# Kernel tuning notes

Measured on AMD Instinct MI355X. Metric: run time of the kernel, lower is better.

Reference implementation:

```python
import jax, jax.numpy as jnp
import numpy as np

U, I, D, E = 8192, 8192, 64, 1048576  # users, items, emb dim, nnz of adjacency


def spmm(row, col, val, x, n):
    """Sparse (COO) @ dense: y[r] += val * x[c], like torch.sparse.mm."""
    return jax.ops.segment_sum(val[:, None] * x[col], row, num_segments=n)


def setup_inputs() -> dict:
    key = jax.random.key(0)
    k1, k2, k3, k4, k5, k6 = jax.random.split(key, 6)
    users_emb = jax.random.normal(k1, (U, D), dtype=jnp.float32) * 0.1  # nn.init.normal_(std=0.1)
    items_emb = jax.random.normal(k2, (I, D), dtype=jnp.float32) * 0.1
    edge_row = jax.random.randint(k3, (E,), 0, U + I, dtype=jnp.int32)
    edge_col = jax.random.randint(k4, (E,), 0, U + I, dtype=jnp.int32)
    # positive normalized adjacency values (stand-in for D^-1/2 A D^-1/2 entries)
    edge_val = jax.random.uniform(k5, (E,), dtype=jnp.float32) / 64.0
    # sparse 0/1 interaction matrix densified, as in labels = interaction_mat.toarray()
    labels = (jax.random.uniform(k6, (U, I)) < 0.02).astype(jnp.float32)
    return {"users_emb": users_emb, "items_emb": items_emb,
            "edge_row": edge_row, "edge_col": edge_col,
            "edge_val": edge_val, "labels": labels, "n_layers": 3}


def reference(users_emb, items_emb, edge_row, edge_col, edge_val, labels, n_layers):
    n = users_emb.shape[0] + items_emb.shape[0]
    u = users_emb.shape[0]
    all_emb = jnp.concatenate([users_emb, items_emb], axis=0)  # [n, D]
    # stack + mean over (n_layers+1) layer outputs == online accumulation
    acc = all_emb
    for _ in range(n_layers):
        all_emb = spmm(edge_row, edge_col, edge_val, all_emb, n)
        acc = acc + all_emb
    light_out = acc / jnp.float32(n_layers + 1)
    user_emb = light_out[:u]   # [U, D]
    item_emb = light_out[u:]   # [I, D]
    scores = user_emb @ item_emb.T  # [U, I]
    # BCEWithLogitsLoss (mean reduction): logaddexp(0, s) - s*y
    loss = jnp.mean(jnp.logaddexp(jnp.float32(0.0), scores) - scores * labels)
    return (loss, user_emb, item_emb)
```

## Files before the change

### kernel.cpp

```cpp
#include <hip/hip_runtime.h>

#define U_N 8192
#define N_N 16384
#define E_N 1048576
#define CAP 128
#define CSTRIDE 16

typedef __attribute__((ext_vector_type(8)))  short short8;
typedef __attribute__((ext_vector_type(16))) float f32x16;


__device__ __forceinline__ float bfu(ushort u) {
    union { unsigned v; float f; } c; c.v = (unsigned)u << 16; return c.f;
}
__device__ __forceinline__ ushort f2bf(float f) {
    union { float f; unsigned u; } c; c.f = f;
    return (ushort)((c.u + 0x7fffu + ((c.u >> 16) & 1u)) >> 16);
}
__device__ __forceinline__ void gload_lds16(const void* g, void* l) {
    __builtin_amdgcn_global_load_lds(
        (const __attribute__((address_space(1))) void*)g,
        (__attribute__((address_space(3))) void*)l, 16, 0, 0);
}

__global__ void k_prep(const float* __restrict__ ue, const float* __restrict__ ie,
                       ushort* __restrict__ xb, float* __restrict__ acc,
                       unsigned* __restrict__ cnt) {
    int i = blockIdx.x * blockDim.x + threadIdx.x;
    const int HU = U_N * 64 / 4;
    float4 v = (i < HU) ? ((const float4*)ue)[i] : ((const float4*)ie)[i - HU];
    ((float4*)acc)[i] = v;
    ushort4 b;
    b.x = f2bf(v.x); b.y = f2bf(v.y); b.z = f2bf(v.z); b.w = f2bf(v.w);
    ((ushort4*)xb)[i] = b;
    if (i < 65536) ((uint4*)cnt)[i] = make_uint4(0, 0, 0, 0);
}

__global__ void k_bucket(const int* __restrict__ row, const int* __restrict__ col,
                         const float* __restrict__ val, unsigned* __restrict__ cnt,
                         int2* __restrict__ buckets) {
    int e = blockIdx.x * blockDim.x + threadIdx.x;
    if (e < E_N) {
        int r = row[e];
        unsigned p = atomicAdd(&cnt[r * CSTRIDE], 1u);
        if (p < CAP) buckets[(size_t)r * CAP + p] = make_int2(col[e], __float_as_int(val[e]));
    }
}

__global__ void k_spmm(const unsigned* __restrict__ cnt, const int4* __restrict__ bk4,
                       const ushort* __restrict__ x, ushort* __restrict__ xo,
                       float* __restrict__ acc) {
    int wave = (int)((blockIdx.x * blockDim.x + threadIdx.x) >> 6);
    int lane = threadIdx.x & 63;
    if (wave >= N_N) return;
    int n = (int)cnt[wave * CSTRIDE]; n = n > CAP ? CAP : n;
    const int4* bp = bk4 + (size_t)wave * (CAP / 2);
    float a = 0.f;
    int j = 0;
    for (; j + 8 <= n; j += 8) {
        int4 q0 = bp[j / 2 + 0], q1 = bp[j / 2 + 1];
        int4 q2 = bp[j / 2 + 2], q3 = bp[j / 2 + 3];
        float x0 = bfu(x[q0.x * 64 + lane]), x1 = bfu(x[q0.z * 64 + lane]);
        float x2 = bfu(x[q1.x * 64 + lane]), x3 = bfu(x[q1.z * 64 + lane]);
        float x4 = bfu(x[q2.x * 64 + lane]), x5 = bfu(x[q2.z * 64 + lane]);
        float x6 = bfu(x[q3.x * 64 + lane]), x7 = bfu(x[q3.z * 64 + lane]);
        a = fmaf(__int_as_float(q0.y), x0, a); a = fmaf(__int_as_float(q0.w), x1, a);
        a = fmaf(__int_as_float(q1.y), x2, a); a = fmaf(__int_as_float(q1.w), x3, a);
        a = fmaf(__int_as_float(q2.y), x4, a); a = fmaf(__int_as_float(q2.w), x5, a);
        a = fmaf(__int_as_float(q3.y), x6, a); a = fmaf(__int_as_float(q3.w), x7, a);
    }
    const int2* bp2 = (const int2*)bp;
    for (; j < n; ++j) {
        int2 q = bp2[j];
        a = fmaf(__int_as_float(q.y), bfu(x[q.x * 64 + lane]), a);
    }
    int idx = wave * 64 + lane;
    xo[idx] = f2bf(a);
    acc[idx] += a;
}

__global__ void k_spmm_last(const unsigned* __restrict__ cnt, const int4* __restrict__ bk4,
                            const ushort* __restrict__ x, const float* __restrict__ acc,
                            float* __restrict__ o, ushort* __restrict__ bfemb) {
    int wave = (int)((blockIdx.x * blockDim.x + threadIdx.x) >> 6);
    int lane = threadIdx.x & 63;
    if (wave >= N_N) return;
    int n = (int)cnt[wave * CSTRIDE]; n = n > CAP ? CAP : n;
    const int4* bp = bk4 + (size_t)wave * (CAP / 2);
    float a = 0.f;
    int j = 0;
    for (; j + 8 <= n; j += 8) {
        int4 q0 = bp[j / 2 + 0], q1 = bp[j / 2 + 1];
        int4 q2 = bp[j / 2 + 2], q3 = bp[j / 2 + 3];
        float x0 = bfu(x[q0.x * 64 + lane]), x1 = bfu(x[q0.z * 64 + lane]);
        float x2 = bfu(x[q1.x * 64 + lane]), x3 = bfu(x[q1.z * 64 + lane]);
        float x4 = bfu(x[q2.x * 64 + lane]), x5 = bfu(x[q2.z * 64 + lane]);
        float x6 = bfu(x[q3.x * 64 + lane]), x7 = bfu(x[q3.z * 64 + lane]);
        a = fmaf(__int_as_float(q0.y), x0, a); a = fmaf(__int_as_float(q0.w), x1, a);
        a = fmaf(__int_as_float(q1.y), x2, a); a = fmaf(__int_as_float(q1.w), x3, a);
        a = fmaf(__int_as_float(q2.y), x4, a); a = fmaf(__int_as_float(q2.w), x5, a);
        a = fmaf(__int_as_float(q3.y), x6, a); a = fmaf(__int_as_float(q3.w), x7, a);
    }
    const int2* bp2 = (const int2*)bp;
    for (; j < n; ++j) {
        int2 q = bp2[j];
        a = fmaf(__int_as_float(q.y), bfu(x[q.x * 64 + lane]), a);
    }
    int idx = wave * 64 + lane;
    float l = (acc[idx] + a) * 0.25f;
    o[idx] = l;
    bfemb[idx] = f2bf(l);
}

__global__ __launch_bounds__(256) void k_gemm_loss(const ushort* __restrict__ bfemb,
                                                   const float* __restrict__ labels,
                                                   float* __restrict__ partials) {
    __shared__ float lab[128 * 128];
    int tid  = threadIdx.x;
    int lane = tid & 63;
    int w    = tid >> 6;
    int wr   = w >> 1, wc = w & 1;
    int row0t = blockIdx.y * 128, col0t = blockIdx.x * 128;
    int row0 = row0t + wr * 64;
    int col0 = col0t + wc * 64;

    {
        int colo = (lane & 31) * 4;
        int rowo = lane >> 5;
        const float* gbase = labels + (size_t)row0t * 8192 + col0t + colo;
        #pragma unroll
        for (int t = 0; t < 16; ++t) {
            int cid = w * 16 + t;
            gload_lds16(gbase + (size_t)(cid * 2 + rowo) * 8192, &lab[cid * 256]);
        }
    }

    int lrow = lane & 31;
    int lk   = (lane >> 5) * 8;
    short8 a[2][4], b[2][4];
    #pragma unroll
    for (int fi = 0; fi < 2; ++fi) {
        const ushort* pa = bfemb + (size_t)(row0 + fi * 32 + lrow) * 64 + lk;
        const ushort* pb = bfemb + (size_t)(U_N + col0 + fi * 32 + lrow) * 64 + lk;
        #pragma unroll
        for (int kk = 0; kk < 4; ++kk) {
            a[fi][kk] = *(const short8*)(pa + kk * 16);
            b[fi][kk] = *(const short8*)(pb + kk * 16);
        }
    }

    f32x16 acc00 = {}, acc01 = {}, acc10 = {}, acc11 = {};
    #pragma unroll
    for (int kk = 0; kk < 4; ++kk) {
        acc00 = __builtin_amdgcn_mfma_f32_32x32x16_bf16(a[0][kk], b[0][kk], acc00, 0, 0, 0);
        acc01 = __builtin_amdgcn_mfma_f32_32x32x16_bf16(a[0][kk], b[1][kk], acc01, 0, 0, 0);
        acc10 = __builtin_amdgcn_mfma_f32_32x32x16_bf16(a[1][kk], b[0][kk], acc10, 0, 0, 0);
        acc11 = __builtin_amdgcn_mfma_f32_32x32x16_bf16(a[1][kk], b[1][kk], acc11, 0, 0, 0);
    }

    asm volatile("s_waitcnt vmcnt(0)" ::: "memory");
    __syncthreads();

    float sum1 = 0.f, sum2 = 0.f, sum4 = 0.f, sumL = 0.f, m2 = 0.f;
    int rsub = (lane >> 5) * 4;
    int lcol = lane & 31;
    #pragma unroll
    for (int fi = 0; fi < 2; ++fi) {
        #pragma unroll
        for (int fj = 0; fj < 2; ++fj) {
            const f32x16& ac = fi ? (fj ? acc11 : acc10) : (fj ? acc01 : acc00);
            int lc = wc * 64 + fj * 32 + lcol;
            int lr0 = wr * 64 + fi * 32 + rsub;
            #pragma unroll
            for (int q = 0; q < 4; ++q) {
                #pragma unroll
                for (int r = 0; r < 4; ++r) {
                    float s = ac[q * 4 + r];
                    float labv = lab[(lr0 + q * 8 + r) * 128 + lc];
                    float s2 = s * s;
                    sum1 += s;
                    sum2 += s2;
                    sum4 = fmaf(s2, s2, sum4);
                    sumL = fmaf(s, labv, sumL);
                    m2 = fmaxf(m2, s2);
                }
            }
        }
    }

    const float LN2 = 0.69314718055994531f;
    float base = fmaf(0.5f, sum1, fmaf(0.125f, sum2, fmaf(-1.f / 192.f, sum4, 64.f * LN2)));

    if (__any(m2 > 1.0f)) {
        base = 0.f;
        #pragma unroll
        for (int fi = 0; fi < 2; ++fi) {
            #pragma unroll
            for (int fj = 0; fj < 2; ++fj) {
                const f32x16& ac = fi ? (fj ? acc11 : acc10) : (fj ? acc01 : acc00);
                #pragma unroll
                for (int t = 0; t < 16; ++t) {
                    float s = ac[t];
                    base += fmaxf(s, 0.f) + __logf(1.f + __expf(-fabsf(s)));
                }
            }
        }
    }

    float sum = base - sumL;
    #pragma unroll
    for (int off = 32; off > 0; off >>= 1) sum += __shfl_down(sum, off);

    __syncthreads();
    volatile float* red = lab;
    if ((tid & 63) == 0) red[w] = sum;
    __syncthreads();
    if (tid == 0)
        partials[blockIdx.y * 64 + blockIdx.x] = red[0] + red[1] + red[2] + red[3];
}

__global__ __launch_bounds__(256) void k_finish(const float* __restrict__ partials,
                                                float* __restrict__ out) {
    __shared__ float red[4];
    int tid = threadIdx.x;
    float s = 0.f;
    #pragma unroll
    for (int t = 0; t < 4; ++t) {
        float4 v = ((const float4*)partials)[tid + t * 256];
        s += (v.x + v.y) + (v.z + v.w);
    }
    #pragma unroll
    for (int off = 32; off > 0; off >>= 1) s += __shfl_down(s, off);
    if ((tid & 63) == 0) red[tid >> 6] = s;
    __syncthreads();
    if (tid == 0) out[0] = (red[0] + red[1] + red[2] + red[3]) * (1.0f / 67108864.0f);
}

extern "C" void kernel_launch(void* const* d_in, const int* in_sizes, int n_in,
                              void* d_out, int out_size, void* d_ws, size_t ws_size,
                              hipStream_t stream) {
    const float* ue     = (const float*)d_in[0];
    const float* ie     = (const float*)d_in[1];
    const int*   erow   = (const int*)d_in[2];
    const int*   ecol   = (const int*)d_in[3];
    const float* eval_  = (const float*)d_in[4];
    const float* labels = (const float*)d_in[5];
    float* out = (float*)d_out;

    char* ws = (char*)d_ws;
    unsigned* cnt      = (unsigned*)(ws + 0);
    float*    partials = (float*)   (ws + 1048576);
    ushort*   xb0      = (ushort*)  (ws + 1081344);
    ushort*   xb1      = (ushort*)  (ws + 3178496);
    float*    accb     = (float*)   (ws + 5275648);
    ushort*   bfemb    = (ushort*)  (ws + 9469952);
    int2*     buckets  = (int2*)    (ws + 11567104);

    k_prep<<<1024, 256, 0, stream>>>(ue, ie, xb0, accb, cnt);
    k_bucket<<<4096, 256, 0, stream>>>(erow, ecol, eval_, cnt, buckets);

    const int4* bk4 = (const int4*)buckets;
    k_spmm<<<4096, 256, 0, stream>>>(cnt, bk4, xb0, xb1, accb);
    k_spmm<<<4096, 256, 0, stream>>>(cnt, bk4, xb1, xb0, accb);
    k_spmm_last<<<4096, 256, 0, stream>>>(cnt, bk4, xb0, accb, out + 1, bfemb);

    dim3 g(64, 64);
    k_gemm_loss<<<g, 256, 0, stream>>>(bfemb, labels, partials);
    k_finish<<<1, 256, 0, stream>>>(partials, out);
}
```

Baseline: 250.3 us.

## Pack labels into bitmask and compress edge records to 32-bit

```diff
diff --git a/kernel.cpp b/kernel.cpp
--- a/kernel.cpp
+++ b/kernel.cpp
@@ -16,11 +16,6 @@
 __device__ __forceinline__ ushort f2bf(float f) {
     union { float f; unsigned u; } c; c.f = f;
     return (ushort)((c.u + 0x7fffu + ((c.u >> 16) & 1u)) >> 16);
-}
-__device__ __forceinline__ void gload_lds16(const void* g, void* l) {
-    __builtin_amdgcn_global_load_lds(
-        (const __attribute__((address_space(1))) void*)g,
-        (__attribute__((address_space(3))) void*)l, 16, 0, 0);
 }
 
 __global__ void k_prep(const float* __restrict__ ue, const float* __restrict__ ie,
@@ -36,76 +31,78 @@
     if (i < 65536) ((uint4*)cnt)[i] = make_uint4(0, 0, 0, 0);
 }
 
+__global__ __launch_bounds__(256) void k_mask(const float* __restrict__ labels,
+                                              unsigned* __restrict__ mask) {
+    int tid = blockIdx.x * 256 + threadIdx.x;
+    const int stride = 2048 * 256;
+    #pragma unroll 4
+    for (int it = 0; it < 32; ++it) {
+        int g = tid + it * stride;
+        float4 v = ((const float4*)labels)[g];
+        unsigned nib = (v.x != 0.f ? 1u : 0u) | (v.y != 0.f ? 2u : 0u)
+                     | (v.z != 0.f ? 4u : 0u) | (v.w != 0.f ? 8u : 0u);
+        unsigned wv = nib << ((g & 7) * 4);
+        wv |= __shfl_xor(wv, 1);
+        wv |= __shfl_xor(wv, 2);
+        wv |= __shfl_xor(wv, 4);
+        if ((threadIdx.x & 7) == 0) mask[g >> 3] = wv;
+    }
+}
+
 __global__ void k_bucket(const int* __restrict__ row, const int* __restrict__ col,
                          const float* __restrict__ val, unsigned* __restrict__ cnt,
-                         int2* __restrict__ buckets) {
+                         unsigned* __restrict__ buckets) {
     int e = blockIdx.x * blockDim.x + threadIdx.x;
     if (e < E_N) {
         int r = row[e];
         unsigned p = atomicAdd(&cnt[r * CSTRIDE], 1u);
-        if (p < CAP) buckets[(size_t)r * CAP + p] = make_int2(col[e], __float_as_int(val[e]));
-    }
-}
-
-__global__ void k_spmm(const unsigned* __restrict__ cnt, const int4* __restrict__ bk4,
+        if (p < CAP)
+            buckets[(size_t)r * CAP + p] = (unsigned)col[e] | ((unsigned)f2bf(val[e]) << 16);
+    }
+}
+
+#define REC_FMA(rec)                                                       \
+    {   unsigned _rc = (rec);                                              \
+        float _xv = bfu(x[(_rc & 0xFFFFu) * 64 + lane]);                   \
+        a = fmaf(bfu((ushort)(_rc >> 16)), _xv, a); }
+
+__global__ void k_spmm(const unsigned* __restrict__ cnt, const unsigned* __restrict__ buckets,
                        const ushort* __restrict__ x, ushort* __restrict__ xo,
                        float* __restrict__ acc) {
     int wave = (int)((blockIdx.x * blockDim.x + threadIdx.x) >> 6);
     int lane = threadIdx.x & 63;
     if (wave >= N_N) return;
     int n = (int)cnt[wave * CSTRIDE]; n = n > CAP ? CAP : n;
-    const int4* bp = bk4 + (size_t)wave * (CAP / 2);
+    const uint4* bp4 = (const uint4*)(buckets + (size_t)wave * CAP);
     float a = 0.f;
     int j = 0;
     for (; j + 8 <= n; j += 8) {
-        int4 q0 = bp[j / 2 + 0], q1 = bp[j / 2 + 1];
-        int4 q2 = bp[j / 2 + 2], q3 = bp[j / 2 + 3];
-        float x0 = bfu(x[q0.x * 64 + lane]), x1 = bfu(x[q0.z * 64 + lane]);
-        float x2 = bfu(x[q1.x * 64 + lane]), x3 = bfu(x[q1.z * 64 + lane]);
-        float x4 = bfu(x[q2.x * 64 + lane]), x5 = bfu(x[q2.z * 64 + lane]);
-        float x6 = bfu(x[q3.x * 64 + lane]), x7 = bfu(x[q3.z * 64 + lane]);
-        a = fmaf(__int_as_float(q0.y), x0, a); a = fmaf(__int_as_float(q0.w), x1, a);
-        a = fmaf(__int_as_float(q1.y), x2, a); a = fmaf(__int_as_float(q1.w), x3, a);
-        a = fmaf(__int_as_float(q2.y), x4, a); a = fmaf(__int_as_float(q2.w), x5, a);
-        a = fmaf(__int_as_float(q3.y), x6, a); a = fmaf(__int_as_float(q3.w), x7, a);
-    }
-    const int2* bp2 = (const int2*)bp;
-    for (; j < n; ++j) {
-        int2 q = bp2[j];
-        a = fmaf(__int_as_float(q.y), bfu(x[q.x * 64 + lane]), a);
-    }
+        uint4 qa = bp4[j >> 2], qb = bp4[(j >> 2) + 1];
+        REC_FMA(qa.x) REC_FMA(qa.y) REC_FMA(qa.z) REC_FMA(qa.w)
+        REC_FMA(qb.x) REC_FMA(qb.y) REC_FMA(qb.z) REC_FMA(qb.w)
+    }
+    for (; j < n; ++j) REC_FMA(buckets[(size_t)wave * CAP + j])
     int idx = wave * 64 + lane;
     xo[idx] = f2bf(a);
     acc[idx] += a;
 }
 
-__global__ void k_spmm_last(const unsigned* __restrict__ cnt, const int4* __restrict__ bk4,
+__global__ void k_spmm_last(const unsigned* __restrict__ cnt, const unsigned* __restrict__ buckets,
                             const ushort* __restrict__ x, const float* __restrict__ acc,
                             float* __restrict__ o, ushort* __restrict__ bfemb) {
     int wave = (int)((blockIdx.x * blockDim.x + threadIdx.x) >> 6);
     int lane = threadIdx.x & 63;
     if (wave >= N_N) return;
     int n = (int)cnt[wave * CSTRIDE]; n = n > CAP ? CAP : n;
-    const int4* bp = bk4 + (size_t)wave * (CAP / 2);
+    const uint4* bp4 = (const uint4*)(buckets + (size_t)wave * CAP);
     float a = 0.f;
     int j = 0;
     for (; j + 8 <= n; j += 8) {
-        int4 q0 = bp[j / 2 + 0], q1 = bp[j / 2 + 1];
-        int4 q2 = bp[j / 2 + 2], q3 = bp[j / 2 + 3];
-        float x0 = bfu(x[q0.x * 64 + lane]), x1 = bfu(x[q0.z * 64 + lane]);
-        float x2 = bfu(x[q1.x * 64 + lane]), x3 = bfu(x[q1.z * 64 + lane]);
-        float x4 = bfu(x[q2.x * 64 + lane]), x5 = bfu(x[q2.z * 64 + lane]);
-        float x6 = bfu(x[q3.x * 64 + lane]), x7 = bfu(x[q3.z * 64 + lane]);
-        a = fmaf(__int_as_float(q0.y), x0, a); a = fmaf(__int_as_float(q0.w), x1, a);
-        a = fmaf(__int_as_float(q1.y), x2, a); a = fmaf(__int_as_float(q1.w), x3, a);
-        a = fmaf(__int_as_float(q2.y), x4, a); a = fmaf(__int_as_float(q2.w), x5, a);
-        a = fmaf(__int_as_float(q3.y), x6, a); a = fmaf(__int_as_float(q3.w), x7, a);
-    }
-    const int2* bp2 = (const int2*)bp;
-    for (; j < n; ++j) {
-        int2 q = bp2[j];
-        a = fmaf(__int_as_float(q.y), bfu(x[q.x * 64 + lane]), a);
-    }
+        uint4 qa = bp4[j >> 2], qb = bp4[(j >> 2) + 1];
+        REC_FMA(qa.x) REC_FMA(qa.y) REC_FMA(qa.z) REC_FMA(qa.w)
+        REC_FMA(qb.x) REC_FMA(qb.y) REC_FMA(qb.z) REC_FMA(qb.w)
+    }
+    for (; j < n; ++j) REC_FMA(buckets[(size_t)wave * CAP + j])
     int idx = wave * 64 + lane;
     float l = (acc[idx] + a) * 0.25f;
     o[idx] = l;
@@ -113,27 +110,21 @@
 }
 
 __global__ __launch_bounds__(256) void k_gemm_loss(const ushort* __restrict__ bfemb,
-                                                   const float* __restrict__ labels,
+                                                   const unsigned* __restrict__ mask,
                                                    float* __restrict__ partials) {
-    __shared__ float lab[128 * 128];
+    __shared__ unsigned lmask[128][4];
+    __shared__ float red[4];
     int tid  = threadIdx.x;
     int lane = tid & 63;
     int w    = tid >> 6;
     int wr   = w >> 1, wc = w & 1;
-    int row0t = blockIdx.y * 128, col0t = blockIdx.x * 128;
+    int row0t = blockIdx.y * 128;
     int row0 = row0t + wr * 64;
-    int col0 = col0t + wc * 64;
-
-    {
-        int colo = (lane & 31) * 4;
-        int rowo = lane >> 5;
-        const float* gbase = labels + (size_t)row0t * 8192 + col0t + colo;
-        #pragma unroll
-        for (int t = 0; t < 16; ++t) {
-            int cid = w * 16 + t;
-            gload_lds16(gbase + (size_t)(cid * 2 + rowo) * 8192, &lab[cid * 256]);
-        }
-    }
+    int col0 = blockIdx.x * 128 + wc * 64;
+
+    if (tid < 128)
+        *(uint4*)&lmask[tid][0] =
+            ((const uint4*)mask)[(size_t)(row0t + tid) * 64 + blockIdx.x];
 
     int lrow = lane & 31;
     int lk   = (lane >> 5) * 8;
@@ -158,25 +149,25 @@
         acc11 = __builtin_amdgcn_mfma_f32_32x32x16_bf16(a[1][kk], b[1][kk], acc11, 0, 0, 0);
     }
 
-    asm volatile("s_waitcnt vmcnt(0)" ::: "memory");
     __syncthreads();
 
     float sum1 = 0.f, sum2 = 0.f, sum4 = 0.f, sumL = 0.f, m2 = 0.f;
     int rsub = (lane >> 5) * 4;
-    int lcol = lane & 31;
+    int bpos = lane & 31;
     #pragma unroll
     for (int fi = 0; fi < 2; ++fi) {
         #pragma unroll
-        for (int fj = 0; fj < 2; ++fj) {
-            const f32x16& ac = fi ? (fj ? acc11 : acc10) : (fj ? acc01 : acc00);
-            int lc = wc * 64 + fj * 32 + lcol;
-            int lr0 = wr * 64 + fi * 32 + rsub;
+        for (int q = 0; q < 4; ++q) {
             #pragma unroll
-            for (int q = 0; q < 4; ++q) {
+            for (int r = 0; r < 4; ++r) {
+                int lr = wr * 64 + fi * 32 + q * 8 + rsub + r;
+                unsigned w0 = lmask[lr][wc * 2 + 0];
+                unsigned w1 = lmask[lr][wc * 2 + 1];
                 #pragma unroll
-                for (int r = 0; r < 4; ++r) {
+                for (int fj = 0; fj < 2; ++fj) {
+                    const f32x16& ac = fi ? (fj ? acc11 : acc10) : (fj ? acc01 : acc00);
                     float s = ac[q * 4 + r];
-                    float labv = lab[(lr0 + q * 8 + r) * 128 + lc];
+                    float labv = (float)(((fj ? w1 : w0) >> bpos) & 1u);
                     float s2 = s * s;
                     sum1 += s;
                     sum2 += s2;
@@ -210,9 +201,6 @@
     float sum = base - sumL;
     #pragma unroll
     for (int off = 32; off > 0; off >>= 1) sum += __shfl_down(sum, off);
-
-    __syncthreads();
-    volatile float* red = lab;
     if ((tid & 63) == 0) red[w] = sum;
     __syncthreads();
     if (tid == 0)
@@ -250,21 +238,22 @@
     char* ws = (char*)d_ws;
     unsigned* cnt      = (unsigned*)(ws + 0);
     float*    partials = (float*)   (ws + 1048576);
-    ushort*   xb0      = (ushort*)  (ws + 1081344);
-    ushort*   xb1      = (ushort*)  (ws + 3178496);
-    float*    accb     = (float*)   (ws + 5275648);
-    ushort*   bfemb    = (ushort*)  (ws + 9469952);
-    int2*     buckets  = (int2*)    (ws + 11567104);
+    unsigned* mask     = (unsigned*)(ws + 1064960);
+    ushort*   xb0      = (ushort*)  (ws + 9453568);
+    ushort*   xb1      = (ushort*)  (ws + 11550720);
+    float*    accb     = (float*)   (ws + 13647872);
+    ushort*   bfemb    = (ushort*)  (ws + 17842176);
+    unsigned* buckets  = (unsigned*)(ws + 19939328);
 
     k_prep<<<1024, 256, 0, stream>>>(ue, ie, xb0, accb, cnt);
     k_bucket<<<4096, 256, 0, stream>>>(erow, ecol, eval_, cnt, buckets);
-
-    const int4* bk4 = (const int4*)buckets;
-    k_spmm<<<4096, 256, 0, stream>>>(cnt, bk4, xb0, xb1, accb);
-    k_spmm<<<4096, 256, 0, stream>>>(cnt, bk4, xb1, xb0, accb);
-    k_spmm_last<<<4096, 256, 0, stream>>>(cnt, bk4, xb0, accb, out + 1, bfemb);
+    k_mask<<<2048, 256, 0, stream>>>(labels, mask);
+
+    k_spmm<<<4096, 256, 0, stream>>>(cnt, buckets, xb0, xb1, accb);
+    k_spmm<<<4096, 256, 0, stream>>>(cnt, buckets, xb1, xb0, accb);
+    k_spmm_last<<<4096, 256, 0, stream>>>(cnt, buckets, xb0, accb, out + 1, bfemb);
 
     dim3 g(64, 64);
-    k_gemm_loss<<<g, 256, 0, stream>>>(bfemb, labels, partials);
+    k_gemm_loss<<<g, 256, 0, stream>>>(bfemb, mask, partials);
     k_finish<<<1, 256, 0, stream>>>(partials, out);
 }
```

Measured after the change: 245.3 us. -2.0%, faster.
